# Kernel optimization log

Measured on AMD Instinct MI355X. Metric: run time of the kernel, lower is better.

## Reference

```python
import jax, jax.numpy as jnp
import numpy as np


def _greens(x, k0_raw, amp_raw):
    """Faithful TunableGreens: FFT-domain filtering with per-channel-pair Green's fn.
    NOTE: the source applies fftn over axes (0,1) (batch+H) but ifftn over axes (1,2)
    (H+W); we replicate that exactly."""
    H, W = x.shape[1], x.shape[2]
    k0 = jax.nn.softplus(k0_raw)    # (C, Co, 1, 1)
    amp = jax.nn.softplus(amp_raw)  # (C, Co, 1, 1)
    fy = (2.0 * jnp.pi) * jnp.fft.fftfreq(H, d=1.0).astype(jnp.float32)
    fx = (2.0 * jnp.pi) * jnp.fft.fftfreq(W, d=1.0).astype(jnp.float32)
    p = fy[:, None] ** 2 + fx[None, :] ** 2            # (H, W) = sum(freq_grid**2, -1)
    g_fourier = 1.0 / (amp * p - k0 - 1j)              # (C, Co, H, W) complex64
    u_fft = jnp.fft.fftn(x, axes=(0, 1))               # axes (0,1) as in source
    u_filtered = jnp.einsum('bijc,coij->bijo', u_fft, g_fourier)
    return jnp.fft.ifftn(u_filtered, axes=(1, 2)).real


def _D(Wm, x):
    # per-pixel channel mixing: x [b,i,j,c], Wm [b,i,j,c,o]
    return jnp.einsum('bijc,bijco->bijo', x, Wm)


def _project(k, W1, b1, W2, b2, W3, b3):
    act = lambda z: jnp.exp(-z ** 2)
    x = act(k @ W1 + b1)
    x = act(x @ W2 + b2)
    return x @ W3 + b3


def setup_inputs() -> dict:
    key = jax.random.key(0)
    ks = jax.random.split(key, 10)
    B, H, W, C = 2, 128, 128, 32
    d = {}
    d['u'] = jax.random.normal(ks[0], (B, H, W, C), jnp.float32)
    d['k'] = jax.random.normal(ks[1], (B, H, W, 1), jnp.float32)
    for i, n in enumerate(['g1', 'g2', 'g3', 'g4']):
        d[n] = jax.random.normal(ks[2 + i], (B, H, W, C, C), jnp.float32) * 0.1
    # Project MLP params (lecun-normal-ish scaling)
    d['W1'] = jax.random.normal(ks[6], (1, C), jnp.float32)
    d['b1'] = jnp.zeros((C,), jnp.float32)
    d['W2'] = jax.random.normal(ks[7], (C, C), jnp.float32) * (1.0 / np.sqrt(C))
    d['b2'] = jnp.zeros((C,), jnp.float32)
    d['W3'] = jax.random.normal(ks[8], (C, C), jnp.float32) * (1.0 / np.sqrt(C))
    d['b3'] = jnp.zeros((C,), jnp.float32)
    # TunableGreens params, constant(1.0) init as in source
    d['k0_G'] = jnp.ones((C, C, 1, 1), jnp.float32)
    d['amp_G'] = jnp.ones((C, C, 1, 1), jnp.float32)
    d['k0_Gs'] = jnp.ones((C, C, 1, 1), jnp.float32)
    d['amp_Gs'] = jnp.ones((C, C, 1, 1), jnp.float32)
    return d


def reference(u, k, g1, g2, g3, g4, W1, b1, W2, b2, W3, b3,
              k0_G, amp_G, k0_Gs, amp_Gs):
    s = _project(k, W1, b1, W2, b2, W3, b3)           # [B,H,W,C]
    u1 = _D(g4, _greens(s, k0_Gs, amp_Gs))
    u2 = _D(g1, _greens(_D(g2, u), k0_G, amp_G)) + _D(g3, u)
    return u1 + u2
```

## Files before the change

kernel.cpp:

```cpp
#include <hip/hip_runtime.h>

using u16 = unsigned short;
using u32 = unsigned int;

#define PI2 6.283185307179586f

struct cpx { float x, y; };

__device__ __forceinline__ float bf2f(u16 h){ return __uint_as_float(((u32)h) << 16); }
__device__ __forceinline__ u16 f2bf(float f){
  u32 u = __float_as_uint(f);
  u = u + 0x7fffu + ((u >> 16) & 1u);
  return (u16)(u >> 16);
}

__device__ __forceinline__ float ldv(const void* base, size_t i, int md){
  return md ? ((const float*)base)[i] : bf2f(((const u16*)base)[i]);
}

__device__ __forceinline__ cpx cadd(cpx a, cpx b){ return {a.x+b.x, a.y+b.y}; }
__device__ __forceinline__ cpx csub(cpx a, cpx b){ return {a.x-b.x, a.y-b.y}; }
__device__ __forceinline__ cpx cmul(cpx a, cpx b){ return {a.x*b.x - a.y*b.y, a.x*b.y + a.y*b.x}; }
__device__ __forceinline__ int br6(int l){ return (int)(__brev((u32)l) >> 26); }
__device__ __forceinline__ cpx shflx(cpx v, int m){
  cpx r; r.x = __shfl_xor(v.x, m, 64); r.y = __shfl_xor(v.y, m, 64); return r;
}

__device__ __forceinline__ void make_tw(int l, cpx tw[6]){
  #pragma unroll
  for (int s = 0; s < 6; s++){
    int h = 64 >> s;
    float ang = -PI2 * (float)(l & (h-1)) / (float)(2*h);
    float sv, cv; sincosf(ang, &sv, &cv);
    tw[s] = {cv, sv};
  }
}

__device__ __forceinline__ void fft_fwd(cpx& v0, cpx& v1, int l, const cpx tw[6]){
  cpx a = cadd(v0, v1), b = csub(v0, v1);
  v0 = a; v1 = cmul(b, tw[0]);
  #pragma unroll
  for (int s = 1; s < 6; s++){
    int h = 64 >> s;
    cpx p0 = shflx(v0, h), p1 = shflx(v1, h);
    bool up = (l & h) != 0;
    cpx n0 = up ? cmul(csub(p0, v0), tw[s]) : cadd(v0, p0);
    cpx n1 = up ? cmul(csub(p1, v1), tw[s]) : cadd(v1, p1);
    v0 = n0; v1 = n1;
  }
  { cpx p0 = shflx(v0, 1), p1 = shflx(v1, 1);
    bool up = (l & 1) != 0;
    v0 = up ? csub(p0, v0) : cadd(v0, p0);
    v1 = up ? csub(p1, v1) : cadd(v1, p1); }
}

__device__ __forceinline__ void fft_inv(cpx& v0, cpx& v1, int l, const cpx tw[6]){
  { cpx p0 = shflx(v0, 1), p1 = shflx(v1, 1);
    bool up = (l & 1) != 0;
    v0 = up ? csub(p0, v0) : cadd(v0, p0);
    v1 = up ? csub(p1, v1) : cadd(v1, p1); }
  #pragma unroll
  for (int s = 5; s >= 1; s--){
    int h = 64 >> s;
    cpx twc = {tw[s].x, -tw[s].y};
    cpx p0 = shflx(v0, h), p1 = shflx(v1, h);
    bool up = (l & h) != 0;
    cpx t0 = cmul(up ? v0 : p0, twc);
    cpx t1 = cmul(up ? v1 : p1, twc);
    v0 = up ? csub(p0, t0) : cadd(v0, t0);
    v1 = up ? csub(p1, t1) : cadd(v1, t1);
  }
  { cpx twc = {tw[0].x, -tw[0].y};
    cpx t = cmul(v1, twc);
    cpx n0 = cadd(v0, t), n1 = csub(v0, t);
    v0 = n0; v1 = n1; }
}

__device__ __forceinline__ float softplusf(float x){ return (x > 20.0f) ? x : log1pf(expf(x)); }

__global__ void k_detect(const void* g1, int* flag){
  __shared__ int cnt;
  if (threadIdx.x == 0) cnt = 0;
  __syncthreads();
  const u16* p = (const u16*)g1;
  int local = 0;
  for (int i = threadIdx.x; i < 4096; i += 256){
    float v = bf2f(p[i]);
    if (!(fabsf(v) < 100.0f)) local++;
  }
  atomicAdd(&cnt, local);
  __syncthreads();
  if (threadIdx.x == 0) *flag = (cnt > 64) ? 1 : 0;
}

__global__ void k_tabs(const void* k0G, const void* ampG, const void* k0Gs, const void* ampGs,
                       float* tabs, const int* flag){
  int md = *flag;
  for (int i = threadIdx.x; i < 1024; i += 256){
    tabs[i]        = softplusf(ldv(ampGs, i, md));
    tabs[1024 + i] = softplusf(ldv(k0Gs, i, md));
    tabs[2048 + i] = softplusf(ldv(ampG, i, md));
    tabs[3072 + i] = softplusf(ldv(k0G, i, md));
  }
}

__global__ __launch_bounds__(256) void k_project(const void* kin, const void* W1, const void* b1,
    const void* W2, const void* b2, const void* W3, const void* b3, float* S, const int* flag){
  __shared__ float sW2[1024], sW3[1024], sml[128];
  int md = *flag;
  int t = threadIdx.x;
  for (int i = t; i < 1024; i += 256){ sW2[i] = ldv(W2, i, md); sW3[i] = ldv(W3, i, md); }
  if (t < 32){
    sml[t]     = ldv(W1, t, md); sml[32+t] = ldv(b1, t, md);
    sml[64+t]  = ldv(b2, t, md); sml[96+t] = ldv(b3, t, md);
  }
  __syncthreads();
  int pix = blockIdx.x * 256 + t;
  float kv = ldv(kin, pix, md);
  float a1[32], a2[32];
  #pragma unroll
  for (int c = 0; c < 32; c++){ float z = fmaf(kv, sml[c], sml[32+c]); a1[c] = expf(-z*z); }
  for (int o = 0; o < 32; o++){
    float z = sml[64+o];
    #pragma unroll
    for (int c = 0; c < 32; c++) z = fmaf(a1[c], sW2[c*32+o], z);
    a2[o] = expf(-z*z);
  }
  for (int o = 0; o < 32; o++){
    float sv = sml[96+o];
    #pragma unroll
    for (int c = 0; c < 32; c++) sv = fmaf(a2[c], sW3[c*32+o], sv);
    S[(size_t)pix*32 + o] = sv;
  }
}

__device__ __forceinline__ void matvec_acc(const void* gbase, size_t pix, float xv, int l, int md, float acc[4]){
  int oq = l & 7, hh = l >> 3;
  if (md){
    const float4* Mv = (const float4*)((const float*)gbase + pix*1024);
    #pragma unroll
    for (int cc = 0; cc < 4; cc++){
      int c = hh*4 + cc;
      float4 m = Mv[c*8 + oq];
      float xc = __shfl(xv, c, 64);
      acc[0] = fmaf(xc, m.x, acc[0]);
      acc[1] = fmaf(xc, m.y, acc[1]);
      acc[2] = fmaf(xc, m.z, acc[2]);
      acc[3] = fmaf(xc, m.w, acc[3]);
    }
  } else {
    const uint2* Mv = (const uint2*)((const u16*)gbase + pix*1024);
    #pragma unroll
    for (int cc = 0; cc < 4; cc++){
      int c = hh*4 + cc;
      uint2 m = Mv[c*8 + oq];
      float xc = __shfl(xv, c, 64);
      acc[0] = fmaf(xc, __uint_as_float(m.x << 16), acc[0]);
      acc[1] = fmaf(xc, __uint_as_float(m.x & 0xffff0000u), acc[1]);
      acc[2] = fmaf(xc, __uint_as_float(m.y << 16), acc[2]);
      acc[3] = fmaf(xc, __uint_as_float(m.y & 0xffff0000u), acc[3]);
    }
  }
}
__device__ __forceinline__ void reduce8(float acc[4]){
  #pragma unroll
  for (int d = 8; d <= 32; d <<= 1){
    acc[0] += __shfl_xor(acc[0], d, 64);
    acc[1] += __shfl_xor(acc[1], d, 64);
    acc[2] += __shfl_xor(acc[2], d, 64);
    acc[3] += __shfl_xor(acc[3], d, 64);
  }
}

__global__ __launch_bounds__(256) void k_dmat(const void* u, const void* g2, float* D, const int* flag){
  int md = *flag;
  int l = threadIdx.x & 63;
  size_t pix = blockIdx.x * 4 + (threadIdx.x >> 6);
  float xu = ldv(u, pix*32 + (l & 31), md);
  float acc[4] = {0.f, 0.f, 0.f, 0.f};
  matvec_acc(g2, pix, xu, l, md, acc);
  reduce8(acc);
  if (l < 8){
    float4 o4 = {acc[0], acc[1], acc[2], acc[3]};
    ((float4*)(D + pix*32))[l] = o4;
  }
}

__global__ __launch_bounds__(256) void kg_a(const float* S, const float* Dd, const float* tabs, float2* Q){
  __shared__ __align__(16) cpx E[64*128];
  int t = threadIdx.x;
  int p = blockIdx.x >> 7, j = blockIdx.x & 127;
  const float* X = p ? Dd : S;
  const float* ampT = tabs + p*2048;
  const float* k0T  = ampT + 1024;
  int l = t & 63, w = t >> 6;
  cpx tw[6]; make_tw(l, tw);

  {
    int h = t >> 1, ch = (t & 1)*16;
    const float4* x0 = (const float4*)(X + (((size_t)h)*128 + j)*32 + ch);
    const float4* x1 = (const float4*)(X + (((size_t)(128 + h))*128 + j)*32 + ch);
    #pragma unroll
    for (int q = 0; q < 4; q++){
      float4 A = x0[q], B = x1[q];
      int c = ch + q*4;
      E[(c+0)*128 + h] = {A.x+B.x, 0.f};  E[(32+c+0)*128 + h] = {A.x-B.x, 0.f};
      E[(c+1)*128 + h] = {A.y+B.y, 0.f};  E[(32+c+1)*128 + h] = {A.y-B.y, 0.f};
      E[(c+2)*128 + h] = {A.z+B.z, 0.f};  E[(32+c+2)*128 + h] = {A.z-B.z, 0.f};
      E[(c+3)*128 + h] = {A.w+B.w, 0.f};  E[(32+c+3)*128 + h] = {A.w-B.w, 0.f};
    }
  }
  __syncthreads();
  for (int c = w; c < 64; c += 4){
    cpx* col = E + c*128;
    cpx v0 = col[l], v1 = col[l+64];
    fft_fwd(v0, v1, l, tw);
    ((float4*)col)[br6(l)] = make_float4(v0.x, v0.y, v1.x, v1.y);
  }
  __syncthreads();
  {
    int o = t & 31, ig = t >> 5;
    float aT[32], kT[32];
    #pragma unroll
    for (int c = 0; c < 32; c++){ aT[c] = ampT[c*32+o]; kT[c] = k0T[c*32+o]; }
    float fj = (j < 64) ? (float)j : (float)(j - 128);
    fj *= (PI2 / 128.0f);
    float px = fj * fj;
    for (int chunk = 0; chunk < 4; chunk++){
      cpx y0[4], y1[4];
      #pragma unroll
      for (int q = 0; q < 4; q++){
        int i = ig + 8*(chunk*4 + q);
        float fi = (i < 64) ? (float)i : (float)(i - 128);
        fi *= (PI2 / 128.0f);
        float pp = fmaf(fi, fi, px);
        cpx a0 = {0.f, 0.f}, a1 = {0.f, 0.f};
        #pragma unroll
        for (int c = 0; c < 32; c++){
          float dd  = fmaf(aT[c], pp, -kT[c]);
          float inv = 1.0f / fmaf(dd, dd, 1.0f);
          float gr = dd * inv, gi = inv;
          cpx x0 = E[c*128 + i];
          cpx x1 = E[(32+c)*128 + i];
          a0.x = fmaf(x0.x, gr, fmaf(-x0.y, gi, a0.x));
          a0.y = fmaf(x0.x, gi, fmaf( x0.y, gr, a0.y));
          a1.x = fmaf(x1.x, gr, fmaf(-x1.y, gi, a1.x));
          a1.y = fmaf(x1.x, gi, fmaf( x1.y, gr, a1.y));
        }
        y0[q] = a0; y1[q] = a1;
      }
      __syncthreads();
      #pragma unroll
      for (int q = 0; q < 4; q++){
        int i = ig + 8*(chunk*4 + q);
        E[o*128 + i]      = y0[q];
        E[(32+o)*128 + i] = y1[q];
      }
      __syncthreads();
    }
  }
  for (int cidx = w; cidx < 64; cidx += 4){
    cpx* col = E + cidx*128;
    float4 tv = ((const float4*)col)[br6(l)];
    cpx v0 = {tv.x, tv.y}, v1 = {tv.z, tv.w};
    fft_inv(v0, v1, l, tw);
    const float sc = 1.0f/128.0f;
    col[l]    = {v0.x*sc, v0.y*sc};
    col[l+64] = {v1.x*sc, v1.y*sc};
  }
  __syncthreads();
  {
    int o = t & 31, bb = (t >> 5) & 1, yb = t >> 6;
    for (int m = 0; m < 32; m++){
      int y = yb + 4*m;
      cpx v = E[(bb*32+o)*128 + y];
      Q[((((size_t)(p*2+bb))*128 + y)*128 + j)*32 + o] = make_float2(v.x, v.y);
    }
  }
}

__global__ __launch_bounds__(256) void kg_c(const float2* Q, float* G0, float* G1){
  __shared__ __align__(16) cpx Z[32*128];
  __shared__ float R[32*128];
  int t = threadIdx.x, l = t & 63, w = t >> 6;
  int idx = blockIdx.x;
  int p = idx >> 8, rem = idx & 255, bb = rem >> 7, y = rem & 127;
  cpx tw[6]; make_tw(l, tw);
  const float4* src = (const float4*)(Q + ((size_t)((p*2+bb)*128 + y))*4096);
  for (int q = t; q < 2048; q += 256){
    float4 v = src[q];
    int m = q*2, jj = m >> 5, c = m & 31;
    Z[c*128 + jj]     = {v.x, v.y};
    Z[(c+1)*128 + jj] = {v.z, v.w};
  }
  __syncthreads();
  for (int c = w; c < 32; c += 4){
    cpx* col = Z + c*128;
    float4 tv = ((const float4*)col)[br6(l)];
    cpx v0 = {tv.x, tv.y}, v1 = {tv.z, tv.w};
    fft_inv(v0, v1, l, tw);
    R[c*128 + l]      = v0.x * (1.0f/128.0f);
    R[c*128 + l + 64] = v1.x * (1.0f/128.0f);
  }
  __syncthreads();
  float* dst = (p ? G1 : G0) + ((size_t)(bb*128 + y))*4096;
  int jj = t >> 3, c4 = (t & 7)*4;
  for (int rep = 0; rep < 4; rep++){
    int j2 = jj + rep*32;
    float4 o4 = { R[(c4+0)*128 + j2], R[(c4+1)*128 + j2],
                  R[(c4+2)*128 + j2], R[(c4+3)*128 + j2] };
    ((float4*)(dst + (size_t)j2*32))[c4 >> 2] = o4;
  }
}

__global__ __launch_bounds__(256) void k_final(const void* u, const void* g1, const void* g3, const void* g4,
    const float* G0, const float* G1, void* out, const int* flag){
  int md = *flag;
  int l = threadIdx.x & 63;
  size_t pix = blockIdx.x * 4 + (threadIdx.x >> 6);
  int c0 = l & 31;
  float xs = G0[pix*32 + c0];
  float xm = G1[pix*32 + c0];
  float xu = ldv(u, pix*32 + c0, md);
  float acc[4] = {0.f, 0.f, 0.f, 0.f};
  matvec_acc(g4, pix, xs, l, md, acc);
  matvec_acc(g1, pix, xm, l, md, acc);
  matvec_acc(g3, pix, xu, l, md, acc);
  reduce8(acc);
  if (l < 8){
    if (md){
      float4 o4 = {acc[0], acc[1], acc[2], acc[3]};
      ((float4*)out)[pix*8 + l] = o4;
    } else {
      u32 lo = (u32)f2bf(acc[0]) | ((u32)f2bf(acc[1]) << 16);
      u32 hi = (u32)f2bf(acc[2]) | ((u32)f2bf(acc[3]) << 16);
      uint2 v = {lo, hi};
      ((uint2*)out)[pix*8 + l] = v;
    }
  }
}

extern "C" void kernel_launch(void* const* d_in, const int* in_sizes, int n_in,
                              void* d_out, int out_size, void* d_ws, size_t ws_size,
                              hipStream_t stream){
  (void)in_sizes; (void)n_in; (void)out_size; (void)ws_size;
  const void* u    = d_in[0];
  const void* kk   = d_in[1];
  const void* g1   = d_in[2];
  const void* g2   = d_in[3];
  const void* g3   = d_in[4];
  const void* g4   = d_in[5];
  const void* W1   = d_in[6];
  const void* b1   = d_in[7];
  const void* W2   = d_in[8];
  const void* b2   = d_in[9];
  const void* W3   = d_in[10];
  const void* b3   = d_in[11];
  const void* k0G  = d_in[12];
  const void* ampG = d_in[13];
  const void* k0Gs = d_in[14];
  const void* ampGs= d_in[15];

  float* ws   = (float*)d_ws;
  float* S    = ws;
  float* Dd   = ws + (1u<<20);
  float2* Q   = (float2*)(ws + 2*(1u<<20));
  float* G0   = ws + 6*(1u<<20);
  float* G1b  = ws + 7*(1u<<20);
  float* tabs = ws + 8*(1u<<20);
  int*   flag = (int*)(tabs + 4096);

  k_detect <<<1,    256, 0, stream>>>(g1, flag);
  k_tabs   <<<1,    256, 0, stream>>>(k0G, ampG, k0Gs, ampGs, tabs, flag);
  k_project<<<128,  256, 0, stream>>>(kk, W1, b1, W2, b2, W3, b3, S, flag);
  k_dmat   <<<8192, 256, 0, stream>>>(u, g2, Dd, flag);
  kg_a     <<<256,  256, 0, stream>>>(S, Dd, tabs, Q);
  kg_c     <<<512,  256, 0, stream>>>(Q, G0, G1b);
  k_final  <<<8192, 256, 0, stream>>>(u, g1, g3, g4, G0, G1b, (void*)d_out, flag);
}
```

Baseline: 556.2 us.

## Widen per-lane weight loads in matvec kernels and double kg_a threads

The per-pixel channel-mixing kernels (k_dmat and k_final) now give each lane 16-byte loads covering 8 output columns across two input rows, instead of 8-byte loads for 4 columns. The shuffle reduction now runs over lane strides 4 to 32. k_dmat also handles two pixels per wavefront and launches half as many blocks. The FFT/Green's kernel kg_a moves to 512 threads per block with its loops re-strided, and uses a hardware reciprocal instead of IEEE division. The aim is fewer, wider memory transactions on the bandwidth-bound weight tensors and more parallelism in kg_a. The costs are higher register pressure and slightly less accurate reciprocals.

Result: faster. 536.7 us (-3.5%).

```diff
diff --git a/kernel.cpp b/kernel.cpp
--- a/kernel.cpp
+++ b/kernel.cpp
@@ -78,6 +78,36 @@
 
 __device__ __forceinline__ float softplusf(float x){ return (x > 20.0f) ? x : log1pf(expf(x)); }
 
+__device__ __forceinline__ void acc8_bf(uint4 a, uint4 b, float x0, float x1, float acc[8]){
+  acc[0] = fmaf(x0, __uint_as_float(a.x << 16),         acc[0]);
+  acc[1] = fmaf(x0, __uint_as_float(a.x & 0xffff0000u), acc[1]);
+  acc[2] = fmaf(x0, __uint_as_float(a.y << 16),         acc[2]);
+  acc[3] = fmaf(x0, __uint_as_float(a.y & 0xffff0000u), acc[3]);
+  acc[4] = fmaf(x0, __uint_as_float(a.z << 16),         acc[4]);
+  acc[5] = fmaf(x0, __uint_as_float(a.z & 0xffff0000u), acc[5]);
+  acc[6] = fmaf(x0, __uint_as_float(a.w << 16),         acc[6]);
+  acc[7] = fmaf(x0, __uint_as_float(a.w & 0xffff0000u), acc[7]);
+  acc[0] = fmaf(x1, __uint_as_float(b.x << 16),         acc[0]);
+  acc[1] = fmaf(x1, __uint_as_float(b.x & 0xffff0000u), acc[1]);
+  acc[2] = fmaf(x1, __uint_as_float(b.y << 16),         acc[2]);
+  acc[3] = fmaf(x1, __uint_as_float(b.y & 0xffff0000u), acc[3]);
+  acc[4] = fmaf(x1, __uint_as_float(b.z << 16),         acc[4]);
+  acc[5] = fmaf(x1, __uint_as_float(b.z & 0xffff0000u), acc[5]);
+  acc[6] = fmaf(x1, __uint_as_float(b.w << 16),         acc[6]);
+  acc[7] = fmaf(x1, __uint_as_float(b.w & 0xffff0000u), acc[7]);
+}
+__device__ __forceinline__ void acc8_f32(float4 a0, float4 a1, float4 b0, float4 b1,
+                                         float x0, float x1, float acc[8]){
+  acc[0] = fmaf(x0, a0.x, acc[0]); acc[1] = fmaf(x0, a0.y, acc[1]);
+  acc[2] = fmaf(x0, a0.z, acc[2]); acc[3] = fmaf(x0, a0.w, acc[3]);
+  acc[4] = fmaf(x0, a1.x, acc[4]); acc[5] = fmaf(x0, a1.y, acc[5]);
+  acc[6] = fmaf(x0, a1.z, acc[6]); acc[7] = fmaf(x0, a1.w, acc[7]);
+  acc[0] = fmaf(x1, b0.x, acc[0]); acc[1] = fmaf(x1, b0.y, acc[1]);
+  acc[2] = fmaf(x1, b0.z, acc[2]); acc[3] = fmaf(x1, b0.w, acc[3]);
+  acc[4] = fmaf(x1, b1.x, acc[4]); acc[5] = fmaf(x1, b1.y, acc[5]);
+  acc[6] = fmaf(x1, b1.z, acc[6]); acc[7] = fmaf(x1, b1.w, acc[7]);
+}
+
 __global__ void k_detect(const void* g1, int* flag){
   __shared__ int cnt;
   if (threadIdx.x == 0) cnt = 0;
@@ -134,59 +164,51 @@
   }
 }
 
-__device__ __forceinline__ void matvec_acc(const void* gbase, size_t pix, float xv, int l, int md, float acc[4]){
-  int oq = l & 7, hh = l >> 3;
-  if (md){
-    const float4* Mv = (const float4*)((const float*)gbase + pix*1024);
-    #pragma unroll
-    for (int cc = 0; cc < 4; cc++){
-      int c = hh*4 + cc;
-      float4 m = Mv[c*8 + oq];
-      float xc = __shfl(xv, c, 64);
-      acc[0] = fmaf(xc, m.x, acc[0]);
-      acc[1] = fmaf(xc, m.y, acc[1]);
-      acc[2] = fmaf(xc, m.z, acc[2]);
-      acc[3] = fmaf(xc, m.w, acc[3]);
-    }
-  } else {
-    const uint2* Mv = (const uint2*)((const u16*)gbase + pix*1024);
-    #pragma unroll
-    for (int cc = 0; cc < 4; cc++){
-      int c = hh*4 + cc;
-      uint2 m = Mv[c*8 + oq];
-      float xc = __shfl(xv, c, 64);
-      acc[0] = fmaf(xc, __uint_as_float(m.x << 16), acc[0]);
-      acc[1] = fmaf(xc, __uint_as_float(m.x & 0xffff0000u), acc[1]);
-      acc[2] = fmaf(xc, __uint_as_float(m.y << 16), acc[2]);
-      acc[3] = fmaf(xc, __uint_as_float(m.y & 0xffff0000u), acc[3]);
-    }
-  }
-}
-__device__ __forceinline__ void reduce8(float acc[4]){
-  #pragma unroll
-  for (int d = 8; d <= 32; d <<= 1){
-    acc[0] += __shfl_xor(acc[0], d, 64);
-    acc[1] += __shfl_xor(acc[1], d, 64);
-    acc[2] += __shfl_xor(acc[2], d, 64);
-    acc[3] += __shfl_xor(acc[3], d, 64);
-  }
-}
-
 __global__ __launch_bounds__(256) void k_dmat(const void* u, const void* g2, float* D, const int* flag){
   int md = *flag;
-  int l = threadIdx.x & 63;
-  size_t pix = blockIdx.x * 4 + (threadIdx.x >> 6);
-  float xu = ldv(u, pix*32 + (l & 31), md);
-  float acc[4] = {0.f, 0.f, 0.f, 0.f};
-  matvec_acc(g2, pix, xu, l, md, acc);
-  reduce8(acc);
-  if (l < 8){
-    float4 o4 = {acc[0], acc[1], acc[2], acc[3]};
-    ((float4*)(D + pix*32))[l] = o4;
-  }
-}
-
-__global__ __launch_bounds__(256) void kg_a(const float* S, const float* Dd, const float* tabs, float2* Q){
+  int t = threadIdx.x, l = t & 63;
+  size_t pix = (size_t)blockIdx.x * 8 + (size_t)(t >> 6) * 2;
+  int c32 = l & 31, ch = l >> 2;
+  float xa = ldv(u, pix*32 + c32, md);
+  float xb = ldv(u, (pix+1)*32 + c32, md);
+  float acc0[8] = {0.f,0.f,0.f,0.f,0.f,0.f,0.f,0.f};
+  float acc1[8] = {0.f,0.f,0.f,0.f,0.f,0.f,0.f,0.f};
+  if (md){
+    const float4* Ra = (const float4*)((const float*)g2 + pix*1024);
+    const float4* Rb = (const float4*)((const float*)g2 + (pix+1)*1024);
+    float4 aa = Ra[2*l], ab = Ra[2*l+1], ac = Ra[128+2*l], ad = Ra[128+2*l+1];
+    float4 ba = Rb[2*l], bb = Rb[2*l+1], bc = Rb[128+2*l], bd = Rb[128+2*l+1];
+    float xa0 = __shfl(xa, ch, 64), xa1 = __shfl(xa, 16+ch, 64);
+    float xb0 = __shfl(xb, ch, 64), xb1 = __shfl(xb, 16+ch, 64);
+    acc8_f32(aa, ab, ac, ad, xa0, xa1, acc0);
+    acc8_f32(ba, bb, bc, bd, xb0, xb1, acc1);
+  } else {
+    const uint4* Ra = (const uint4*)((const u16*)g2 + pix*1024);
+    const uint4* Rb = (const uint4*)((const u16*)g2 + (pix+1)*1024);
+    uint4 a0 = Ra[l], a1 = Ra[64+l];
+    uint4 b0 = Rb[l], b1 = Rb[64+l];
+    float xa0 = __shfl(xa, ch, 64), xa1 = __shfl(xa, 16+ch, 64);
+    float xb0 = __shfl(xb, ch, 64), xb1 = __shfl(xb, 16+ch, 64);
+    acc8_bf(a0, a1, xa0, xa1, acc0);
+    acc8_bf(b0, b1, xb0, xb1, acc1);
+  }
+  #pragma unroll
+  for (int d = 4; d <= 32; d <<= 1){
+    #pragma unroll
+    for (int jj = 0; jj < 8; jj++){
+      acc0[jj] += __shfl_xor(acc0[jj], d, 64);
+      acc1[jj] += __shfl_xor(acc1[jj], d, 64);
+    }
+  }
+  if (l < 4){
+    ((float4*)(D + pix*32))[2*l]       = make_float4(acc0[0], acc0[1], acc0[2], acc0[3]);
+    ((float4*)(D + pix*32))[2*l+1]     = make_float4(acc0[4], acc0[5], acc0[6], acc0[7]);
+    ((float4*)(D + (pix+1)*32))[2*l]   = make_float4(acc1[0], acc1[1], acc1[2], acc1[3]);
+    ((float4*)(D + (pix+1)*32))[2*l+1] = make_float4(acc1[4], acc1[5], acc1[6], acc1[7]);
+  }
+}
+
+__global__ __launch_bounds__(512) void kg_a(const float* S, const float* Dd, const float* tabs, float2* Q){
   __shared__ __align__(16) cpx E[64*128];
   int t = threadIdx.x;
   int p = blockIdx.x >> 7, j = blockIdx.x & 127;
@@ -197,11 +219,11 @@
   cpx tw[6]; make_tw(l, tw);
 
   {
-    int h = t >> 1, ch = (t & 1)*16;
+    int h = t >> 2, ch = (t & 3) * 8;
     const float4* x0 = (const float4*)(X + (((size_t)h)*128 + j)*32 + ch);
     const float4* x1 = (const float4*)(X + (((size_t)(128 + h))*128 + j)*32 + ch);
     #pragma unroll
-    for (int q = 0; q < 4; q++){
+    for (int q = 0; q < 2; q++){
       float4 A = x0[q], B = x1[q];
       int c = ch + q*4;
       E[(c+0)*128 + h] = {A.x+B.x, 0.f};  E[(32+c+0)*128 + h] = {A.x-B.x, 0.f};
@@ -211,7 +233,7 @@
     }
   }
   __syncthreads();
-  for (int c = w; c < 64; c += 4){
+  for (int c = w; c < 64; c += 8){
     cpx* col = E + c*128;
     cpx v0 = col[l], v1 = col[l+64];
     fft_fwd(v0, v1, l, tw);
@@ -226,11 +248,11 @@
     float fj = (j < 64) ? (float)j : (float)(j - 128);
     fj *= (PI2 / 128.0f);
     float px = fj * fj;
-    for (int chunk = 0; chunk < 4; chunk++){
+    for (int chunk = 0; chunk < 2; chunk++){
       cpx y0[4], y1[4];
       #pragma unroll
       for (int q = 0; q < 4; q++){
-        int i = ig + 8*(chunk*4 + q);
+        int i = ig + 16*(chunk*4 + q);
         float fi = (i < 64) ? (float)i : (float)(i - 128);
         fi *= (PI2 / 128.0f);
         float pp = fmaf(fi, fi, px);
@@ -238,7 +260,7 @@
         #pragma unroll
         for (int c = 0; c < 32; c++){
           float dd  = fmaf(aT[c], pp, -kT[c]);
-          float inv = 1.0f / fmaf(dd, dd, 1.0f);
+          float inv = __builtin_amdgcn_rcpf(fmaf(dd, dd, 1.0f));
           float gr = dd * inv, gi = inv;
           cpx x0 = E[c*128 + i];
           cpx x1 = E[(32+c)*128 + i];
@@ -252,14 +274,14 @@
       __syncthreads();
       #pragma unroll
       for (int q = 0; q < 4; q++){
-        int i = ig + 8*(chunk*4 + q);
+        int i = ig + 16*(chunk*4 + q);
         E[o*128 + i]      = y0[q];
         E[(32+o)*128 + i] = y1[q];
       }
       __syncthreads();
     }
   }
-  for (int cidx = w; cidx < 64; cidx += 4){
+  for (int cidx = w; cidx < 64; cidx += 8){
     cpx* col = E + cidx*128;
     float4 tv = ((const float4*)col)[br6(l)];
     cpx v0 = {tv.x, tv.y}, v1 = {tv.z, tv.w};
@@ -271,8 +293,8 @@
   __syncthreads();
   {
     int o = t & 31, bb = (t >> 5) & 1, yb = t >> 6;
-    for (int m = 0; m < 32; m++){
-      int y = yb + 4*m;
+    for (int m = 0; m < 16; m++){
+      int y = yb + 8*m;
       cpx v = E[(bb*32+o)*128 + y];
       Q[((((size_t)(p*2+bb))*128 + y)*128 + j)*32 + o] = make_float2(v.x, v.y);
     }
@@ -316,26 +338,58 @@
 __global__ __launch_bounds__(256) void k_final(const void* u, const void* g1, const void* g3, const void* g4,
     const float* G0, const float* G1, void* out, const int* flag){
   int md = *flag;
-  int l = threadIdx.x & 63;
-  size_t pix = blockIdx.x * 4 + (threadIdx.x >> 6);
-  int c0 = l & 31;
-  float xs = G0[pix*32 + c0];
-  float xm = G1[pix*32 + c0];
-  float xu = ldv(u, pix*32 + c0, md);
-  float acc[4] = {0.f, 0.f, 0.f, 0.f};
-  matvec_acc(g4, pix, xs, l, md, acc);
-  matvec_acc(g1, pix, xm, l, md, acc);
-  matvec_acc(g3, pix, xu, l, md, acc);
-  reduce8(acc);
-  if (l < 8){
+  int t = threadIdx.x, l = t & 63;
+  size_t pix = (size_t)blockIdx.x * 4 + (t >> 6);
+  int c32 = l & 31, ch = l >> 2;
+  float xs = G0[pix*32 + c32];
+  float xm = G1[pix*32 + c32];
+  float xu = ldv(u, pix*32 + c32, md);
+  float acc[8] = {0.f,0.f,0.f,0.f,0.f,0.f,0.f,0.f};
+  if (md){
+    const float4* R4 = (const float4*)((const float*)g4 + pix*1024);
+    const float4* R1 = (const float4*)((const float*)g1 + pix*1024);
+    const float4* R3 = (const float4*)((const float*)g3 + pix*1024);
+    float4 p4a = R4[2*l], p4b = R4[2*l+1], q4a = R4[128+2*l], q4b = R4[128+2*l+1];
+    float4 p1a = R1[2*l], p1b = R1[2*l+1], q1a = R1[128+2*l], q1b = R1[128+2*l+1];
+    float4 p3a = R3[2*l], p3b = R3[2*l+1], q3a = R3[128+2*l], q3b = R3[128+2*l+1];
+    float xs0 = __shfl(xs, ch, 64), xs1 = __shfl(xs, 16+ch, 64);
+    float xm0 = __shfl(xm, ch, 64), xm1 = __shfl(xm, 16+ch, 64);
+    float xu0 = __shfl(xu, ch, 64), xu1 = __shfl(xu, 16+ch, 64);
+    acc8_f32(p4a, p4b, q4a, q4b, xs0, xs1, acc);
+    acc8_f32(p1a, p1b, q1a, q1b, xm0, xm1, acc);
+    acc8_f32(p3a, p3b, q3a, q3b, xu0, xu1, acc);
+  } else {
+    const uint4* R4 = (const uint4*)((const u16*)g4 + pix*1024);
+    const uint4* R1 = (const uint4*)((const u16*)g1 + pix*1024);
+    const uint4* R3 = (const uint4*)((const u16*)g3 + pix*1024);
+    uint4 a4 = R4[l], b4 = R4[64+l];
+    uint4 a1 = R1[l], b1 = R1[64+l];
+    uint4 a3 = R3[l], b3 = R3[64+l];
+    float xs0 = __shfl(xs, ch, 64), xs1 = __shfl(xs, 16+ch, 64);
+    float xm0 = __shfl(xm, ch, 64), xm1 = __shfl(xm, 16+ch, 64);
+    float xu0 = __shfl(xu, ch, 64), xu1 = __shfl(xu, 16+ch, 64);
+    acc8_bf(a4, b4, xs0, xs1, acc);
+    acc8_bf(a1, b1, xm0, xm1, acc);
+    acc8_bf(a3, b3, xu0, xu1, acc);
+  }
+  #pragma unroll
+  for (int d = 4; d <= 32; d <<= 1){
+    #pragma unroll
+    for (int jj = 0; jj < 8; jj++) acc[jj] += __shfl_xor(acc[jj], d, 64);
+  }
+  if (l < 4){
     if (md){
-      float4 o4 = {acc[0], acc[1], acc[2], acc[3]};
-      ((float4*)out)[pix*8 + l] = o4;
+      float4 o0 = {acc[0], acc[1], acc[2], acc[3]};
+      float4 o1 = {acc[4], acc[5], acc[6], acc[7]};
+      ((float4*)out)[pix*8 + 2*l]     = o0;
+      ((float4*)out)[pix*8 + 2*l + 1] = o1;
     } else {
-      u32 lo = (u32)f2bf(acc[0]) | ((u32)f2bf(acc[1]) << 16);
-      u32 hi = (u32)f2bf(acc[2]) | ((u32)f2bf(acc[3]) << 16);
-      uint2 v = {lo, hi};
-      ((uint2*)out)[pix*8 + l] = v;
+      uint4 v;
+      v.x = (u32)f2bf(acc[0]) | ((u32)f2bf(acc[1]) << 16);
+      v.y = (u32)f2bf(acc[2]) | ((u32)f2bf(acc[3]) << 16);
+      v.z = (u32)f2bf(acc[4]) | ((u32)f2bf(acc[5]) << 16);
+      v.w = (u32)f2bf(acc[6]) | ((u32)f2bf(acc[7]) << 16);
+      ((uint4*)out)[pix*4 + l] = v;
     }
   }
 }
@@ -373,8 +427,8 @@
   k_detect <<<1,    256, 0, stream>>>(g1, flag);
   k_tabs   <<<1,    256, 0, stream>>>(k0G, ampG, k0Gs, ampGs, tabs, flag);
   k_project<<<128,  256, 0, stream>>>(kk, W1, b1, W2, b2, W3, b3, S, flag);
-  k_dmat   <<<8192, 256, 0, stream>>>(u, g2, Dd, flag);
-  kg_a     <<<256,  256, 0, stream>>>(S, Dd, tabs, Q);
+  k_dmat   <<<4096, 256, 0, stream>>>(u, g2, Dd, flag);
+  kg_a     <<<256,  512, 0, stream>>>(S, Dd, tabs, Q);
   kg_c     <<<512,  256, 0, stream>>>(Q, G0, G1b);
   k_final  <<<8192, 256, 0, stream>>>(u, g1, g3, g4, G0, G1b, (void*)d_out, flag);
 }
```
